# Performance work log

Measured on AMD Instinct MI355X. Metric: run time of the kernel, lower is better.

## Reference

```python
import jax, jax.numpy as jnp
import numpy as np


def _haar_dwt(x):
    # pywt 'haar' dwt2 on even-sized inputs: non-overlapping 2x2 blocks.
    # For block [[a,b],[c,d]]: cA=(a+b+c+d)/2, cH=(a+b-c-d)/2,
    # cV=(a-b+c-d)/2, cD=(a-b-c+d)/2  (pywt dec_hi = [-1/sqrt2, 1/sqrt2]).
    B, C, H, W = x.shape
    xb = x.reshape(B, C, H // 2, 2, W // 2, 2)
    a = xb[:, :, :, 0, :, 0]
    b = xb[:, :, :, 0, :, 1]
    c = xb[:, :, :, 1, :, 0]
    d = xb[:, :, :, 1, :, 1]
    ll = (a + b + c + d) * 0.5
    ch = (a + b - c - d) * 0.5
    cv = (a - b + c - d) * 0.5
    cd = (a - b - c + d) * 0.5
    return ll, ch, cv, cd


def _haar_idwt(ll, ch, cv, cd):
    a = (ll + ch + cv + cd) * 0.5
    b = (ll + ch - cv - cd) * 0.5
    c = (ll - ch + cv - cd) * 0.5
    d = (ll - ch - cv + cd) * 0.5
    B, C, h2, w2 = ll.shape
    top = jnp.stack([a, b], axis=-1)   # [B,C,h2,w2,2]
    bot = jnp.stack([c, d], axis=-1)   # [B,C,h2,w2,2]
    y = jnp.stack([top, bot], axis=-3)  # [B,C,h2,2,w2,2]
    return y.reshape(B, C, 2 * h2, 2 * w2)


def _conv2d(x, w, b, groups=1, pad=1):
    y = jax.lax.conv_general_dilated(
        x, w, window_strides=(1, 1), padding=[(pad, pad), (pad, pad)],
        dimension_numbers=('NCHW', 'OIHW', 'NCHW'), feature_group_count=groups)
    return y + b[None, :, None, None]


def setup_inputs() -> dict:
    key = jax.random.key(0)
    ks = jax.random.split(key, 7)
    B, C, H, W = 8, 64, 256, 256
    C4 = 4 * C
    x = jax.random.normal(ks[0], (B, C, H, W), dtype=jnp.float32)
    dw_w = jax.random.normal(ks[1], (C4, 1, 3, 3), dtype=jnp.float32) / 3.0
    dw_b = jax.random.normal(ks[2], (C4,), dtype=jnp.float32) * 0.01
    pw_w = jax.random.normal(ks[3], (C4, C4, 1, 1), dtype=jnp.float32) / float(np.sqrt(C4))
    pw_b = jax.random.normal(ks[4], (C4,), dtype=jnp.float32) * 0.01
    cv_w = jax.random.normal(ks[5], (C4, C4, 3, 3), dtype=jnp.float32) / float(3.0 * np.sqrt(C4))
    cv_b = jax.random.normal(ks[6], (C4,), dtype=jnp.float32) * 0.01
    return {"x": x, "dw_w": dw_w, "dw_b": dw_b, "pw_w": pw_w,
            "pw_b": pw_b, "cv_w": cv_w, "cv_b": cv_b}


def reference(x, dw_w, dw_b, pw_w, pw_b, cv_w, cv_b):
    B, C, H, W = x.shape  # source math requires H == W (spatial transpose)
    C4 = 4 * C
    ll, ch, cv, cd = _haar_dwt(x)
    # Source stores each subband spatially TRANSPOSED (transpose(2,1,0)).
    sub = jnp.stack([jnp.swapaxes(s, -1, -2) for s in (ll, ch, cv, cd)], axis=2)
    t = sub.reshape(B, C4, H // 2, W // 2)  # channel order c*4 + {LL,cH,cV,cD}
    t = _conv2d(t, dw_w, dw_b, groups=C4, pad=1)  # depthwise 3x3
    t = _conv2d(t, pw_w, pw_b, groups=1, pad=0)   # pointwise 1x1
    t = _conv2d(t, cv_w, cv_b, groups=1, pad=1)   # dense 3x3
    t = jax.nn.gelu(t, approximate=False)         # torch nn.GELU() = exact erf
    t = t.reshape(B, C, 4, H // 2, W // 2)
    # Inverse path un-transposes each subband (transpose(0,2) in source).
    ll2, ch2, cv2, cd2 = [jnp.swapaxes(t[:, :, k], -1, -2) for k in range(4)]
    return _haar_idwt(ll2, ch2, cv2, cd2)
```

## Files before the change

### kernel.cpp

```cpp
#include <hip/hip_runtime.h>
#include <hip/hip_bf16.h>

#define DEVI __device__ __forceinline__

typedef __attribute__((ext_vector_type(8))) short abf8;
typedef __attribute__((ext_vector_type(4))) float f32x4;

DEVI unsigned short f2bf(float f) {
  union { __hip_bfloat16 h; unsigned short u; } cvt;
  cvt.h = __float2bfloat16(f);
  return cvt.u;
}
DEVI float bf2f(unsigned short u) {
  return __uint_as_float(((unsigned)u) << 16);
}
DEVI void async16(const void* g, void* l) {
  __builtin_amdgcn_global_load_lds((__attribute__((address_space(1))) void*)(g),
                                   (__attribute__((address_space(3))) void*)(l), 16, 0, 0);
}

__global__ __launch_bounds__(256) void k0_prep(const float* __restrict__ pw_w,
                                               const float* __restrict__ cv_w,
                                               unsigned short* __restrict__ pwb,
                                               unsigned short* __restrict__ cvb) {
  int id = blockIdx.x * 256 + threadIdx.x;
  if (id < 65536) pwb[id] = f2bf(pw_w[id]);
  if (id < 589824) {
    int dd = id >> 16;
    int rem = id & 65535;
    cvb[id] = f2bf(cv_w[(size_t)rem * 9 + dd]);
  }
}

__global__ __launch_bounds__(256) void k1a_dwt(const float* __restrict__ x,
                                               unsigned short* __restrict__ t0) {
  __shared__ __align__(16) float L[64 * 65];
  const int t = threadIdx.x;
  const int u0 = (blockIdx.x & 3) * 32;
  const int v0 = (blockIdx.x >> 2) * 32;
  const int c = blockIdx.y, b = blockIdx.z;
  const float* xp = x + (((size_t)(b * 64 + c)) << 16);
  {
    const int row = t >> 2;
    const float* xr = xp + (size_t)(2 * v0 + row) * 256 + 2 * u0;
    float* Lr = L + row * 65;
    for (int j = 0; j < 4; ++j) {
      int col = ((t & 3) + j * 4) * 4;
      float4 val = *(const float4*)(xr + col);
      Lr[col] = val.x; Lr[col + 1] = val.y; Lr[col + 2] = val.z; Lr[col + 3] = val.w;
    }
  }
  __syncthreads();
  const int vv = t & 31;
  const int us = t >> 5;
  const size_t outc = ((size_t)(b * 256 + c * 4)) << 14;
  for (int pass = 0; pass < 4; ++pass) {
    int uu = us * 4 + pass;
    const float* Lp = L + (2 * vv) * 65 + 2 * uu;
    float a = Lp[0], bb = Lp[1], cc = Lp[65], dd = Lp[66];
    float sll = (a + bb + cc + dd) * 0.5f;
    float sch = (a + bb - cc - dd) * 0.5f;
    float scv = (a - bb + cc - dd) * 0.5f;
    float scd = (a - bb - cc + dd) * 0.5f;
    size_t base = outc + ((u0 + uu) << 7) + (v0 + vv);
    t0[base]         = f2bf(sll);
    t0[base + 16384] = f2bf(sch);
    t0[base + 32768] = f2bf(scv);
    t0[base + 49152] = f2bf(scd);
  }
}

__global__ __launch_bounds__(256) void k1b_dw(const unsigned short* __restrict__ t0,
                                              const float* __restrict__ dww,
                                              const float* __restrict__ dwb,
                                              unsigned short* __restrict__ t1) {
  __shared__ __align__(16) unsigned short S[32 * 181];
  __shared__ __align__(16) unsigned short O[128 * 32];
  const int t = threadIdx.x;
  const int u0 = (blockIdx.x >> 3) * 8;
  const int v0 = (blockIdx.x & 7) * 16;
  const int icB = blockIdx.y * 32;
  const int b = blockIdx.z;
  const unsigned short* t0b = t0 + (((size_t)(b * 256 + icB)) << 14);
  for (int idx = t; idx < 5760; idx += 256) {
    int ic = idx / 180;
    int r = idx - ic * 180;
    int uu = r / 18;
    int vvq = r - uu * 18;
    int gu = u0 + uu - 1, gv = v0 + vvq - 1;
    unsigned short val = 0;
    if ((unsigned)gu < 128u && (unsigned)gv < 128u)
      val = t0b[((size_t)ic << 14) + (gu << 7) + gv];
    S[ic * 181 + r] = val;
  }
  __syncthreads();
  const int icp = t & 15, uu = (t >> 4) & 7, vh = t >> 7;
  const int cc0 = icB + icp * 2;
  float w0[9], w1[9];
  const float* wp = dww + cc0 * 9;
  for (int i = 0; i < 9; ++i) { w0[i] = wp[i]; w1[i] = wp[9 + i]; }
  const float b0 = dwb[cc0], b1 = dwb[cc0 + 1];
  const unsigned short* S0 = S + (icp * 2) * 181 + uu * 18 + vh * 8;
  const unsigned short* S1 = S0 + 181;
  float a0[3][3], a1[3][3];
  for (int du = 0; du < 3; ++du)
    for (int dv = 0; dv < 2; ++dv) {
      a0[du][dv] = bf2f(S0[du * 18 + dv]);
      a1[du][dv] = bf2f(S1[du * 18 + dv]);
    }
  unsigned* O32 = (unsigned*)O;
  for (int vv = 0; vv < 8; ++vv) {
    for (int du = 0; du < 3; ++du) {
      a0[du][2] = bf2f(S0[du * 18 + vv + 2]);
      a1[du][2] = bf2f(S1[du * 18 + vv + 2]);
    }
    float s0 = b0, s1 = b1;
    for (int du = 0; du < 3; ++du)
      for (int dv = 0; dv < 3; ++dv) {
        s0 += w0[du * 3 + dv] * a0[du][dv];
        s1 += w1[du * 3 + dv] * a1[du][dv];
      }
    int p = uu * 16 + vh * 8 + vv;
    O32[p * 16 + icp] = (unsigned)f2bf(s0) | ((unsigned)f2bf(s1) << 16);
    for (int du = 0; du < 3; ++du) {
      a0[du][0] = a0[du][1]; a0[du][1] = a0[du][2];
      a1[du][0] = a1[du][1]; a1[du][1] = a1[du][2];
    }
  }
  __syncthreads();
  const int p = t >> 1, hf = t & 1;
  const int pu = p >> 4, pv = p & 15;
  size_t gp = (size_t)((u0 + pu) * 128 + (v0 + pv));
  const uint4* src = (const uint4*)(O + p * 32 + hf * 16);
  uint4* dst = (uint4*)(t1 + ((((size_t)b * 16384) + gp) << 8) + icB + hf * 16);
  dst[0] = src[0];
  dst[1] = src[1];
}

__global__ __launch_bounds__(256) void k2_pw(const unsigned short* __restrict__ t1,
                                             const unsigned short* __restrict__ pwb,
                                             const float* __restrict__ pw_bias,
                                             unsigned short* __restrict__ t2) {
  __shared__ __align__(16) char smem[34816];
  unsigned short* As = (unsigned short*)smem;
  unsigned short* Bs = (unsigned short*)(smem + 8192);
  unsigned short* Ost = (unsigned short*)smem;
  const int t = threadIdx.x;
  const int wv = t >> 6, ln = t & 63;
  const int p0 = blockIdx.x * 128;
  const int oc0 = blockIdx.y * 128;
  const int b = blockIdx.z;
  const unsigned short* t1b = t1 + ((size_t)b << 22);
  const int q = ln >> 4, cl = ln & 15;
  const int lr = ln >> 2, sp = ln & 3;
  const int sc = (sp - (lr >> 1)) & 3;
  const int soff = ((q + (cl >> 1)) & 3) * 8;
  f32x4 acc[2][8] = {};
  for (int ic0 = 0; ic0 < 256; ic0 += 32) {
    __syncthreads();
    for (int cpy = 0; cpy < 2; ++cpy) {
      int rb = wv * 32 + cpy * 16;
      async16(pwb + (((size_t)(oc0 + rb + lr)) << 8) + ic0 + sc * 8, As + rb * 32);
      async16(t1b + (((size_t)(p0 + rb + lr)) << 8) + ic0 + sc * 8, Bs + rb * 32);
    }
    __syncthreads();
    abf8 a0 = *(const abf8*)(As + (wv * 32 + cl) * 32 + soff);
    abf8 a1 = *(const abf8*)(As + (wv * 32 + 16 + cl) * 32 + soff);
    for (int nt = 0; nt < 8; ++nt) {
      abf8 bf = *(const abf8*)(Bs + (nt * 16 + cl) * 32 + soff);
      acc[0][nt] = __builtin_amdgcn_mfma_f32_16x16x32_bf16(a0, bf, acc[0][nt], 0, 0, 0);
      acc[1][nt] = __builtin_amdgcn_mfma_f32_16x16x32_bf16(a1, bf, acc[1][nt], 0, 0, 0);
    }
  }
  __syncthreads();
  for (int mt = 0; mt < 2; ++mt) {
    int ocr = wv * 32 + mt * 16 + q * 4;
    float bb0 = pw_bias[oc0 + ocr],     bb1 = pw_bias[oc0 + ocr + 1];
    float bb2 = pw_bias[oc0 + ocr + 2], bb3 = pw_bias[oc0 + ocr + 3];
    for (int nt = 0; nt < 8; ++nt) {
      int p = nt * 16 + cl;
      short4 pk;
      pk.x = (short)f2bf(acc[mt][nt][0] + bb0);
      pk.y = (short)f2bf(acc[mt][nt][1] + bb1);
      pk.z = (short)f2bf(acc[mt][nt][2] + bb2);
      pk.w = (short)f2bf(acc[mt][nt][3] + bb3);
      *(short4*)(Ost + p * 136 + ocr) = pk;
    }
  }
  __syncthreads();
  const int pr = t >> 1, hf = t & 1;
  const uint4* src = (const uint4*)(Ost + pr * 136 + hf * 64);
  uint4* dst = (uint4*)(t2 + (((size_t)(b * 16384 + p0 + pr)) << 8) + oc0 + hf * 64);
  for (int j = 0; j < 8; ++j) dst[j] = src[j];
}

__global__ __launch_bounds__(256) void k3_cv(const unsigned short* __restrict__ t2,
                                             const unsigned short* __restrict__ cvb,
                                             const float* __restrict__ cv_bias,
                                             unsigned short* __restrict__ t3) {
  __shared__ __align__(16) char smem[34816];
  unsigned short* As = (unsigned short*)smem;
  unsigned short* Bs = (unsigned short*)(smem + 24576);
  unsigned short* Ost = (unsigned short*)smem;
  const int t = threadIdx.x;
  const int wv = t >> 6, ln = t & 63;
  const int oc0 = blockIdx.x * 128;
  const int u = blockIdx.y;
  const int b = blockIdx.z;
  const unsigned short* t2b = t2 + ((size_t)b << 22);
  const int q = ln >> 4, cl = ln & 15;
  const int lr = ln >> 2, sp = ln & 3;
  const int scA = (sp - (lr >> 1)) & 3;
  const int scB = (sp - ((1 + lr) >> 1)) & 3;
  const int soffA = ((q + (cl >> 1)) & 3) * 8;
  if (t < 32) ((unsigned*)Bs)[t < 16 ? t : (2064 + (t - 16))] = 0;
  f32x4 acc[2][8] = {};
  for (int du = 0; du < 3; ++du) {
    const int us = u + du - 1;
    if ((unsigned)us >= 128u) continue;
    const unsigned short* trow = t2b + ((size_t)us << 15);
    const unsigned short* wdu = cvb + (((size_t)(du * 3)) << 16);
    for (int ic0 = 0; ic0 < 256; ic0 += 32) {
      __syncthreads();
      for (int g = wv; g < 32; g += 4) {
        if (g < 24) {
          int dv = g >> 3, ch = g & 7;
          async16(wdu + (((size_t)dv) << 16) + (((size_t)(oc0 + ch * 16 + lr)) << 8) + ic0 + scA * 8,
                  As + dv * 4096 + ch * 512);
        } else {
          int ch = g - 24;
          async16(trow + (((size_t)(ch * 16 + lr)) << 8) + ic0 + scB * 8,
                  Bs + 32 + ch * 512);
        }
      }
      __syncthreads();
      for (int dv = 0; dv < 3; ++dv) {
        const unsigned short* Adv = As + dv * 4096;
        abf8 a0 = *(const abf8*)(Adv + (wv * 32 + cl) * 32 + soffA);
        abf8 a1 = *(const abf8*)(Adv + (wv * 32 + 16 + cl) * 32 + soffA);
        const int slotB = ((q + ((cl + dv) >> 1)) & 3) * 8;
        const unsigned short* Bbase = Bs + (cl + dv) * 32 + slotB;
        for (int nt = 0; nt < 8; ++nt) {
          abf8 bf = *(const abf8*)(Bbase + nt * 512);
          acc[0][nt] = __builtin_amdgcn_mfma_f32_16x16x32_bf16(a0, bf, acc[0][nt], 0, 0, 0);
          acc[1][nt] = __builtin_amdgcn_mfma_f32_16x16x32_bf16(a1, bf, acc[1][nt], 0, 0, 0);
        }
      }
    }
  }
  __syncthreads();
  for (int mt = 0; mt < 2; ++mt) {
    int ocr = wv * 32 + mt * 16 + q * 4;
    for (int r = 0; r < 4; ++r) {
      float bias = cv_bias[oc0 + ocr + r];
      for (int nt = 0; nt < 8; ++nt) {
        float xv = acc[mt][nt][r] + bias;
        float u_ = 0.7978845608028654f * xv * (1.0f + 0.044715f * xv * xv);
        float e = __expf(-2.0f * fabsf(u_));
        float th = (1.0f - e) / (1.0f + e);
        th = (u_ >= 0.0f) ? th : -th;
        float g = 0.5f * xv * (1.0f + th);
        Ost[(ocr + r) * 136 + nt * 16 + cl] = f2bf(g);
      }
    }
  }
  __syncthreads();
  const int rr = t >> 1, hf = t & 1;
  const uint4* src = (const uint4*)(Ost + rr * 136 + hf * 64);
  uint4* dst = (uint4*)(t3 + ((size_t)(b * 256 + oc0 + rr) << 14) + (u << 7) + hf * 64);
  for (int j = 0; j < 8; ++j) dst[j] = src[j];
}

__global__ __launch_bounds__(256) void k4_idwt(const unsigned short* __restrict__ t3,
                                               float* __restrict__ out) {
  __shared__ __align__(16) unsigned short L[4 * 32 * 34];
  const int t = threadIdx.x;
  const int w20 = (blockIdx.x & 3) * 32;
  const int h20 = (blockIdx.x >> 2) * 32;
  const int c = blockIdx.y, b = blockIdx.z;
  const unsigned short* t3b = t3 + (((size_t)(b * 256 + c * 4)) << 14);
  {
    const int row = t >> 1, hf = t & 1;
    const int k = row >> 5, w2i = row & 31;
    const unsigned* g = (const unsigned*)(t3b + ((size_t)k << 14) + ((w20 + w2i) << 7) + h20 + hf * 16);
    unsigned* l = (unsigned*)(L + (k * 32 + w2i) * 34 + hf * 16);
    for (int j = 0; j < 8; ++j) l[j] = g[j];
  }
  __syncthreads();
  const int w2 = t & 31;
  const int h2b = t >> 5;
  float* ob = out + (((size_t)(b * 64 + c)) << 16);
  for (int pass = 0; pass < 4; ++pass) {
    int h2 = h2b + pass * 8;
    int off = w2 * 34 + h2;
    float ll = bf2f(L[off]);
    float ch = bf2f(L[off + 1088]);
    float cv = bf2f(L[off + 2176]);
    float cd = bf2f(L[off + 3264]);
    float A  = (ll + ch + cv + cd) * 0.5f;
    float Bv = (ll + ch - cv - cd) * 0.5f;
    float Cv = (ll - ch + cv - cd) * 0.5f;
    float D  = (ll - ch - cv + cd) * 0.5f;
    int hg = (h20 + h2) * 2, wg = (w20 + w2) * 2;
    *(float2*)(ob + (size_t)hg * 256 + wg)       = make_float2(A, Bv);
    *(float2*)(ob + (size_t)(hg + 1) * 256 + wg) = make_float2(Cv, D);
  }
}

extern "C" void kernel_launch(void* const* d_in, const int* in_sizes, int n_in,
                              void* d_out, int out_size, void* d_ws, size_t ws_size,
                              hipStream_t stream) {
  const float* x    = (const float*)d_in[0];
  const float* dw_w = (const float*)d_in[1];
  const float* dw_b = (const float*)d_in[2];
  const float* pw_w = (const float*)d_in[3];
  const float* pw_b = (const float*)d_in[4];
  const float* cv_w = (const float*)d_in[5];
  const float* cv_b = (const float*)d_in[6];
  char* ws = (char*)d_ws;
  unsigned short* pwb  = (unsigned short*)(ws + 4096);
  unsigned short* cvb  = (unsigned short*)(ws + 4096 + 131072);
  unsigned short* bufA = (unsigned short*)(ws + (size_t)(2u << 20));
  unsigned short* bufB = (unsigned short*)(ws + (size_t)(70u << 20));
  k0_prep<<<2304, 256, 0, stream>>>(pw_w, cv_w, pwb, cvb);
  k1a_dwt<<<dim3(16, 64, 8), 256, 0, stream>>>(x, bufA);
  k1b_dw<<<dim3(128, 8, 8), 256, 0, stream>>>(bufA, dw_w, dw_b, bufB);
  k2_pw<<<dim3(128, 2, 8), 256, 0, stream>>>(bufB, pwb, pw_b, bufA);
  k3_cv<<<dim3(2, 128, 8), 256, 0, stream>>>(bufA, cvb, cv_b, bufB);
  k4_idwt<<<dim3(16, 64, 8), 256, 0, stream>>>(bufB, (float*)d_out);
}
```

Baseline: 594.7 us.

## Fold pointwise 1x1 conv into dense 3x3 conv weights and boundary-aware bias

Result: faster. 563.6 us (-5.2%).

```diff
diff --git a/kernel.cpp b/kernel.cpp
--- a/kernel.cpp
+++ b/kernel.cpp
@@ -19,17 +19,69 @@
                                    (__attribute__((address_space(3))) void*)(l), 16, 0, 0);
 }
 
-__global__ __launch_bounds__(256) void k0_prep(const float* __restrict__ pw_w,
-                                               const float* __restrict__ cv_w,
-                                               unsigned short* __restrict__ pwb,
-                                               unsigned short* __restrict__ cvb) {
-  int id = blockIdx.x * 256 + threadIdx.x;
-  if (id < 65536) pwb[id] = f2bf(pw_w[id]);
-  if (id < 589824) {
-    int dd = id >> 16;
-    int rem = id & 65535;
-    cvb[id] = f2bf(cv_w[(size_t)rem * 9 + dd]);
-  }
+__global__ __launch_bounds__(256) void k0w(const float* __restrict__ cv_w,
+                                           const float* __restrict__ pw_w,
+                                           const float* __restrict__ pw_b,
+                                           unsigned short* __restrict__ cvb,
+                                           float* __restrict__ pb3) {
+  __shared__ __align__(16) unsigned short As[128 * 32];
+  __shared__ __align__(16) unsigned short Bs[128 * 32];
+  const int t = threadIdx.x;
+  const int wv = t >> 6, ln = t & 63, q = ln >> 4, cl = ln & 15;
+  const int dd = blockIdx.x;
+  const int oc0 = blockIdx.y * 128, ic0 = blockIdx.z * 128;
+  f32x4 acc[2][8] = {};
+  float pacc = 0.0f;
+  for (int m0 = 0; m0 < 256; m0 += 32) {
+    __syncthreads();
+    {
+      const int ocr = t >> 1, h = t & 1;
+      const float* src = cv_w + ((size_t)(oc0 + ocr) * 256 + m0 + h * 16) * 9 + dd;
+      unsigned short* dstp = As + ocr * 32 + h * 16;
+      for (int j = 0; j < 16; ++j) dstp[j] = f2bf(src[j * 9]);
+    }
+    for (int idx = t; idx < 4096; idx += 256) {
+      int r = idx >> 7, c = idx & 127;
+      Bs[c * 32 + r] = f2bf(pw_w[(size_t)(m0 + r) * 256 + ic0 + c]);
+    }
+    __syncthreads();
+    if (blockIdx.z == 0 && t < 128) {
+      for (int mk = 0; mk < 32; ++mk) pacc += bf2f(As[t * 32 + mk]) * pw_b[m0 + mk];
+    }
+    abf8 a0 = *(const abf8*)(As + (wv * 32 + cl) * 32 + q * 8);
+    abf8 a1 = *(const abf8*)(As + (wv * 32 + 16 + cl) * 32 + q * 8);
+    for (int nt = 0; nt < 8; ++nt) {
+      abf8 bf = *(const abf8*)(Bs + (nt * 16 + cl) * 32 + q * 8);
+      acc[0][nt] = __builtin_amdgcn_mfma_f32_16x16x32_bf16(a0, bf, acc[0][nt], 0, 0, 0);
+      acc[1][nt] = __builtin_amdgcn_mfma_f32_16x16x32_bf16(a1, bf, acc[1][nt], 0, 0, 0);
+    }
+  }
+  if (blockIdx.z == 0 && t < 128) pb3[(size_t)(oc0 + t) * 9 + dd] = pacc;
+  for (int mt = 0; mt < 2; ++mt)
+    for (int r = 0; r < 4; ++r)
+      for (int nt = 0; nt < 8; ++nt) {
+        int oc = oc0 + wv * 32 + mt * 16 + q * 4 + r;
+        int ic = ic0 + nt * 16 + cl;
+        cvb[((size_t)dd << 16) + oc * 256 + ic] = f2bf(acc[mt][nt][r]);
+      }
+}
+
+__global__ __launch_bounds__(256) void k0q(const float* __restrict__ pb3,
+                                           const float* __restrict__ cv_b,
+                                           float* __restrict__ bias9) {
+  const int oc = threadIdx.x;
+  float p[9];
+  for (int i = 0; i < 9; ++i) p[i] = pb3[oc * 9 + i];
+  const float cb = cv_b[oc];
+  for (int uc = 0; uc < 3; ++uc)
+    for (int vc = 0; vc < 3; ++vc) {
+      int du0 = (uc == 0) ? 1 : 0, du1 = (uc == 2) ? 1 : 2;
+      int dv0 = (vc == 0) ? 1 : 0, dv1 = (vc == 2) ? 1 : 2;
+      float s = cb;
+      for (int du = du0; du <= du1; ++du)
+        for (int dv = dv0; dv <= dv1; ++dv) s += p[du * 3 + dv];
+      bias9[(uc * 3 + vc) * 256 + oc] = s;
+    }
 }
 
 __global__ __launch_bounds__(256) void k1a_dwt(const float* __restrict__ x,
@@ -137,66 +189,9 @@
   dst[1] = src[1];
 }
 
-__global__ __launch_bounds__(256) void k2_pw(const unsigned short* __restrict__ t1,
-                                             const unsigned short* __restrict__ pwb,
-                                             const float* __restrict__ pw_bias,
-                                             unsigned short* __restrict__ t2) {
-  __shared__ __align__(16) char smem[34816];
-  unsigned short* As = (unsigned short*)smem;
-  unsigned short* Bs = (unsigned short*)(smem + 8192);
-  unsigned short* Ost = (unsigned short*)smem;
-  const int t = threadIdx.x;
-  const int wv = t >> 6, ln = t & 63;
-  const int p0 = blockIdx.x * 128;
-  const int oc0 = blockIdx.y * 128;
-  const int b = blockIdx.z;
-  const unsigned short* t1b = t1 + ((size_t)b << 22);
-  const int q = ln >> 4, cl = ln & 15;
-  const int lr = ln >> 2, sp = ln & 3;
-  const int sc = (sp - (lr >> 1)) & 3;
-  const int soff = ((q + (cl >> 1)) & 3) * 8;
-  f32x4 acc[2][8] = {};
-  for (int ic0 = 0; ic0 < 256; ic0 += 32) {
-    __syncthreads();
-    for (int cpy = 0; cpy < 2; ++cpy) {
-      int rb = wv * 32 + cpy * 16;
-      async16(pwb + (((size_t)(oc0 + rb + lr)) << 8) + ic0 + sc * 8, As + rb * 32);
-      async16(t1b + (((size_t)(p0 + rb + lr)) << 8) + ic0 + sc * 8, Bs + rb * 32);
-    }
-    __syncthreads();
-    abf8 a0 = *(const abf8*)(As + (wv * 32 + cl) * 32 + soff);
-    abf8 a1 = *(const abf8*)(As + (wv * 32 + 16 + cl) * 32 + soff);
-    for (int nt = 0; nt < 8; ++nt) {
-      abf8 bf = *(const abf8*)(Bs + (nt * 16 + cl) * 32 + soff);
-      acc[0][nt] = __builtin_amdgcn_mfma_f32_16x16x32_bf16(a0, bf, acc[0][nt], 0, 0, 0);
-      acc[1][nt] = __builtin_amdgcn_mfma_f32_16x16x32_bf16(a1, bf, acc[1][nt], 0, 0, 0);
-    }
-  }
-  __syncthreads();
-  for (int mt = 0; mt < 2; ++mt) {
-    int ocr = wv * 32 + mt * 16 + q * 4;
-    float bb0 = pw_bias[oc0 + ocr],     bb1 = pw_bias[oc0 + ocr + 1];
-    float bb2 = pw_bias[oc0 + ocr + 2], bb3 = pw_bias[oc0 + ocr + 3];
-    for (int nt = 0; nt < 8; ++nt) {
-      int p = nt * 16 + cl;
-      short4 pk;
-      pk.x = (short)f2bf(acc[mt][nt][0] + bb0);
-      pk.y = (short)f2bf(acc[mt][nt][1] + bb1);
-      pk.z = (short)f2bf(acc[mt][nt][2] + bb2);
-      pk.w = (short)f2bf(acc[mt][nt][3] + bb3);
-      *(short4*)(Ost + p * 136 + ocr) = pk;
-    }
-  }
-  __syncthreads();
-  const int pr = t >> 1, hf = t & 1;
-  const uint4* src = (const uint4*)(Ost + pr * 136 + hf * 64);
-  uint4* dst = (uint4*)(t2 + (((size_t)(b * 16384 + p0 + pr)) << 8) + oc0 + hf * 64);
-  for (int j = 0; j < 8; ++j) dst[j] = src[j];
-}
-
-__global__ __launch_bounds__(256) void k3_cv(const unsigned short* __restrict__ t2,
+__global__ __launch_bounds__(256) void k3_cv(const unsigned short* __restrict__ t1,
                                              const unsigned short* __restrict__ cvb,
-                                             const float* __restrict__ cv_bias,
+                                             const float* __restrict__ bias9,
                                              unsigned short* __restrict__ t3) {
   __shared__ __align__(16) char smem[34816];
   unsigned short* As = (unsigned short*)smem;
@@ -207,7 +202,7 @@
   const int oc0 = blockIdx.x * 128;
   const int u = blockIdx.y;
   const int b = blockIdx.z;
-  const unsigned short* t2b = t2 + ((size_t)b << 22);
+  const unsigned short* t1b = t1 + ((size_t)b << 22);
   const int q = ln >> 4, cl = ln & 15;
   const int lr = ln >> 2, sp = ln & 3;
   const int scA = (sp - (lr >> 1)) & 3;
@@ -218,7 +213,7 @@
   for (int du = 0; du < 3; ++du) {
     const int us = u + du - 1;
     if ((unsigned)us >= 128u) continue;
-    const unsigned short* trow = t2b + ((size_t)us << 15);
+    const unsigned short* trow = t1b + ((size_t)us << 15);
     const unsigned short* wdu = cvb + (((size_t)(du * 3)) << 16);
     for (int ic0 = 0; ic0 < 256; ic0 += 32) {
       __syncthreads();
@@ -249,11 +244,21 @@
     }
   }
   __syncthreads();
+  const int uc = (u == 0) ? 0 : ((u == 127) ? 2 : 1);
+  const float* b9 = bias9 + uc * 3 * 256;
+  const bool isv0 = (cl == 0), isv127 = (cl == 15);
   for (int mt = 0; mt < 2; ++mt) {
     int ocr = wv * 32 + mt * 16 + q * 4;
     for (int r = 0; r < 4; ++r) {
-      float bias = cv_bias[oc0 + ocr + r];
+      int ocA = oc0 + ocr + r;
+      float bmid = b9[256 + ocA - oc0 + oc0];
+      float blo  = b9[ocA];
+      float bhi  = b9[512 + ocA];
+      bmid = b9[256 + ocA];
       for (int nt = 0; nt < 8; ++nt) {
+        float bias = bmid;
+        if (nt == 0 && isv0) bias = blo;
+        else if (nt == 7 && isv127) bias = bhi;
         float xv = acc[mt][nt][r] + bias;
         float u_ = 0.7978845608028654f * xv * (1.0f + 0.044715f * xv * xv);
         float e = __expf(-2.0f * fabsf(u_));
@@ -318,14 +323,15 @@
   const float* cv_w = (const float*)d_in[5];
   const float* cv_b = (const float*)d_in[6];
   char* ws = (char*)d_ws;
-  unsigned short* pwb  = (unsigned short*)(ws + 4096);
-  unsigned short* cvb  = (unsigned short*)(ws + 4096 + 131072);
+  float* pb3           = (float*)ws;
+  float* bias9         = (float*)(ws + 16384);
+  unsigned short* cvb  = (unsigned short*)(ws + 65536);
   unsigned short* bufA = (unsigned short*)(ws + (size_t)(2u << 20));
   unsigned short* bufB = (unsigned short*)(ws + (size_t)(70u << 20));
-  k0_prep<<<2304, 256, 0, stream>>>(pw_w, cv_w, pwb, cvb);
+  k0w<<<dim3(9, 2, 2), 256, 0, stream>>>(cv_w, pw_w, pw_b, cvb, pb3);
+  k0q<<<1, 256, 0, stream>>>(pb3, cv_b, bias9);
   k1a_dwt<<<dim3(16, 64, 8), 256, 0, stream>>>(x, bufA);
   k1b_dw<<<dim3(128, 8, 8), 256, 0, stream>>>(bufA, dw_w, dw_b, bufB);
-  k2_pw<<<dim3(128, 2, 8), 256, 0, stream>>>(bufB, pwb, pw_b, bufA);
-  k3_cv<<<dim3(2, 128, 8), 256, 0, stream>>>(bufA, cvb, cv_b, bufB);
-  k4_idwt<<<dim3(16, 64, 8), 256, 0, stream>>>(bufB, (float*)d_out);
-}
+  k3_cv<<<dim3(2, 128, 8), 256, 0, stream>>>(bufB, cvb, bias9, bufA);
+  k4_idwt<<<dim3(16, 64, 8), 256, 0, stream>>>(bufA, (float*)d_out);
+}
```
